# Kernel tuning notes

Measured on AMD Instinct MI355X. Metric: run time of the kernel, lower is better.

Reference implementation:

```python
import jax, jax.numpy as jnp
import numpy as np


def eops_2_to_2(x):
    # x: (N, D, m, m) -> (N, D, 15, m, m), Maron et al. equivariant basis with 'inf' normalization
    m = x.shape[-1]
    fm = float(m)
    eye = jnp.eye(m, dtype=x.dtype)
    diag = jnp.diagonal(x, axis1=-2, axis2=-1)          # (N, D, m)
    sum_diag = diag.sum(-1, keepdims=True)              # (N, D, 1)
    sum_rows = x.sum(-1)                                # (N, D, m) sum over columns j
    sum_cols = x.sum(-2)                                # (N, D, m) sum over rows i
    tot = x.sum((-2, -1))                               # (N, D)

    de = lambda v: v[..., :, None] * eye                # diag_embed (N,D,m) -> (N,D,m,m)
    b_row = lambda v: jnp.broadcast_to(v[..., :, None], v.shape + (m,))           # row i constant = v[i]
    b_col = lambda v: jnp.broadcast_to(v[..., None, :], v.shape[:-1] + (m, m))    # col j constant = v[j]

    op1 = de(diag)
    op2 = de(jnp.broadcast_to(sum_diag, diag.shape)) / fm
    op3 = de(sum_rows) / fm
    op4 = de(sum_cols) / fm
    op5 = de(jnp.broadcast_to(tot[..., None], diag.shape)) / (fm * fm)
    op6 = b_row(sum_cols) / fm
    op7 = b_row(sum_rows) / fm
    op8 = b_col(sum_cols) / fm
    op9 = b_col(sum_rows) / fm
    op10 = x
    op11 = jnp.swapaxes(x, -1, -2)
    op12 = b_row(diag)
    op13 = b_col(diag)
    op14 = jnp.broadcast_to(sum_diag[..., None], x.shape) / fm
    op15 = jnp.broadcast_to(tot[..., None, None], x.shape) / (fm * fm)
    return jnp.stack([op1, op2, op3, op4, op5, op6, op7, op8,
                      op9, op10, op11, op12, op13, op14, op15], axis=2)


def setup_inputs() -> dict:
    key = jax.random.key(0)
    k1, k2 = jax.random.split(key)
    N, D, S, B, m = 32, 32, 32, 15, 128
    std = np.sqrt(2.0 / (D + S + B)).astype(np.float32)
    inputs = jax.random.normal(k1, (N, D, m, m), dtype=jnp.float32)
    coefs = jax.random.normal(k2, (D, S, B), dtype=jnp.float32) * std
    bias = jnp.zeros((1, S, 1, 1), dtype=jnp.float32)
    diag_bias = jnp.zeros((1, S, 1, 1), dtype=jnp.float32)
    return {"inputs": inputs, "coefs": coefs, "bias": bias, "diag_bias": diag_bias}


def reference(inputs, coefs, bias, diag_bias):
    ops = eops_2_to_2(inputs)                               # (N, D, 15, m, m)
    out = jnp.einsum('dsb,ndbij->nsij', coefs, ops)         # (N, S, m, m)
    m = out.shape[-1]
    eye = jnp.eye(m, dtype=out.dtype)[None, None]           # (1,1,m,m)
    return out + bias + eye * diag_bias
```

## Files before the change

### kernel.cpp

```cpp
#include <hip/hip_runtime.h>

#define N_ 32
#define D_ 32
#define S_ 32
#define M_ 128
#define MM_ (M_ * M_)
#define INV_M (1.0f / 128.0f)
#define INV_M2 (1.0f / (128.0f * 128.0f))

typedef float f32x4 __attribute__((ext_vector_type(4)));
typedef __bf16 bf16x8 __attribute__((ext_vector_type(8)));

#define WS_ROWSUM  0
#define WS_COLSUM  131072
#define WS_DIAG    262144
#define WS_SUMDIAG 393216
#define WS_TOT     394240
#define WS_RV      395264
#define WS_CV      526336
#define WS_DG      657408
#define WS_WBF16   788480

__device__ __forceinline__ unsigned short f2bf(float f) {
    unsigned u = __float_as_uint(f);
    u += 0x7fffu + ((u >> 16) & 1u);
    return (unsigned short)(u >> 16);
}

__global__ __launch_bounds__(256) void eq2_reduce(const float* __restrict__ x,
                                                  float* __restrict__ ws) {
    int nd = blockIdx.x;
    int t  = threadIdx.x;
    int g  = t >> 5;
    int j4 = t & 31;

    const float4* xp = (const float4*)(x + (size_t)nd * MM_);

    float* rowsum  = ws + WS_ROWSUM;
    float* colsum  = ws + WS_COLSUM;
    float* diag    = ws + WS_DIAG;
    float* sumdiag = ws + WS_SUMDIAG;
    float* tot     = ws + WS_TOT;

    float4 cs = {0.f, 0.f, 0.f, 0.f};
    float dsum = 0.f, ttot = 0.f;

    for (int r = 0; r < 16; ++r) {
        int i = g * 16 + r;
        float4 v = xp[i * 32 + j4];
        cs.x += v.x; cs.y += v.y; cs.z += v.z; cs.w += v.w;
        float rp = v.x + v.y + v.z + v.w;
        ttot += rp;
        int c = i - 4 * j4;
        if (c >= 0 && c < 4) {
            float dv = (c == 0) ? v.x : (c == 1) ? v.y : (c == 2) ? v.z : v.w;
            diag[nd * M_ + i] = dv;
            dsum += dv;
        }
        float rs = rp;
        for (int msk = 1; msk < 32; msk <<= 1) rs += __shfl_xor(rs, msk, 64);
        if ((t & 31) == 0) rowsum[nd * M_ + i] = rs;
    }

    __shared__ float4 cs_lds[8][32];
    __shared__ float  red[2][4];
    cs_lds[g][j4] = cs;

    for (int msk = 1; msk < 64; msk <<= 1) {
        dsum += __shfl_xor(dsum, msk, 64);
        ttot += __shfl_xor(ttot, msk, 64);
    }
    int wave = t >> 6, lane = t & 63;
    if (lane == 0) { red[0][wave] = dsum; red[1][wave] = ttot; }
    __syncthreads();

    if (t < 32) {
        float4 a = cs_lds[0][t];
        for (int gg = 1; gg < 8; ++gg) {
            float4 b = cs_lds[gg][t];
            a.x += b.x; a.y += b.y; a.z += b.z; a.w += b.w;
        }
        ((float4*)(colsum + nd * M_))[t] = a;
    }
    if (t == 0) {
        sumdiag[nd] = red[0][0] + red[0][1] + red[0][2] + red[0][3];
        tot[nd]     = red[1][0] + red[1][1] + red[1][2] + red[1][3];
    }
}

__global__ __launch_bounds__(128) void eq2_combine(const float* __restrict__ coefs,
                                                   const float* __restrict__ bias,
                                                   const float* __restrict__ diag_bias,
                                                   float* __restrict__ ws) {
    int b = blockIdx.x;
    int n = b >> 5, s = b & 31;
    int i = threadIdx.x;

    const float* rowsum  = ws + WS_ROWSUM;
    const float* colsum  = ws + WS_COLSUM;
    const float* diag    = ws + WS_DIAG;
    const float* sumdiag = ws + WS_SUMDIAG;
    const float* tot     = ws + WS_TOT;

    float rv = 0.f, cv = 0.f, dg = 0.f, kk = 0.f;
    for (int d = 0; d < D_; ++d) {
        const float* cf = coefs + (d * S_ + s) * 15;
        float rs = rowsum[(n * D_ + d) * M_ + i];
        float c2 = colsum[(n * D_ + d) * M_ + i];
        float dv = diag[(n * D_ + d) * M_ + i];
        float sd = sumdiag[n * D_ + d];
        float tt = tot[n * D_ + d];
        rv += (cf[5] * c2 + cf[6] * rs) * INV_M + cf[11] * dv;
        cv += (cf[7] * c2 + cf[8] * rs) * INV_M + cf[12] * dv;
        dg += cf[0] * dv + (cf[1] * sd + cf[2] * rs + cf[3] * c2) * INV_M
              + cf[4] * tt * INV_M2;
        kk += cf[13] * sd * INV_M + cf[14] * tt * INV_M2;
    }
    ws[WS_RV + (n * S_ + s) * M_ + i] = rv + kk + bias[s];
    ws[WS_CV + (n * S_ + s) * M_ + i] = cv;
    ws[WS_DG + (n * S_ + s) * M_ + i] = dg + diag_bias[s];

    if (n == 0 && i < 32) {
        int d = i;
        unsigned short* wsbf = (unsigned short*)(ws + WS_WBF16);
        const float* cf = coefs + (d * S_ + s) * 15;
        wsbf[s * 40 + d]        = f2bf(cf[9]);
        wsbf[(32 + s) * 40 + d] = f2bf(cf[10]);
    }
}

__global__ __launch_bounds__(512, 4) void eq2_main(const float* __restrict__ x,
                                                   const float* __restrict__ ws_,
                                                   float* __restrict__ out) {
    const float* ws = (const float*)__builtin_assume_aligned(ws_, 256);
    int lid = blockIdx.x;
    int n   = (lid & 7) + 8 * (lid >> 8);
    int b   = (lid >> 3) & 31;

    int AR, AC, BR, BC, diagpair;
    if (b < 28) {
        int ti = 0, rem = b;
        while (rem >= 7 - ti) { rem -= 7 - ti; ++ti; }
        int tj = ti + 1 + rem;
        AR = ti * 16; AC = tj * 16;
        BR = tj * 16; BC = ti * 16;
        diagpair = 0;
    } else {
        int p = b - 28;
        AR = AC = (2 * p) * 16;
        BR = BC = (2 * p + 1) * 16;
        diagpair = 1;
    }

    int t    = threadIdx.x;
    int w    = t >> 6;
    int lane = t & 63;
    int lg   = lane >> 4;
    int lj   = lane & 15;

    __shared__ float trf[8 * 545];
    __shared__ float lds_rv[S_][32];
    __shared__ float lds_cv[S_][32];
    __shared__ float lds_dg[S_][32];

    const unsigned short* wsbf = (const unsigned short*)(ws + WS_WBF16);
    const float* xn = x + (size_t)n * (D_ * MM_);

    bf16x8 A10[2], A11[2];
#pragma unroll
    for (int mt = 0; mt < 2; ++mt) {
        A10[mt] = *(const bf16x8*)(wsbf + (mt * 16 + lj) * 40 + lg * 8);
        A11[mt] = *(const bf16x8*)(wsbf + (32 + mt * 16 + lj) * 40 + lg * 8);
    }

    {
        const float* Rv = ws + WS_RV;
        const float* Cv = ws + WS_CV;
        const float* Dg = ws + WS_DG;
#pragma unroll
        for (int k = 0; k < 2; ++k) {
            int idx = k * 512 + t;
            int s = idx >> 5, q = idx & 31;
            int base = (n * S_ + s) * M_;
            int ro = (q < 16) ? AR + q : BR + (q - 16);
            int co = (q < 16) ? AC + q : BC + (q - 16);
            lds_rv[s][q] = Rv[base + ro];
            lds_cv[s][q] = Cv[base + co];
            if (diagpair) lds_dg[s][q] = Dg[base + ro];
        }
    }

    f32x4 aY[4][2], aZ[4][2];
#pragma unroll
    for (int k = 0; k < 4; ++k)
#pragma unroll
        for (int mt = 0; mt < 2; ++mt) { aY[k][mt] = 0.f; aZ[k][mt] = 0.f; }

#pragma unroll
    for (int half = 0; half < 2; ++half) {
        float fv[2][8];
#pragma unroll
        for (int kk = 0; kk < 2; ++kk) {
            int k  = half * 2 + kk;
            int nt = w * 4 + k;
            int tt = nt >> 4, il = nt & 15;
            int Rt = tt ? BR : AR, Ct = tt ? BC : AC;
            const float* src = xn + (Rt + il) * M_ + Ct + lj + (size_t)(lg * 8) * MM_;
#pragma unroll
            for (int e = 0; e < 8; ++e)
                fv[kk][e] = src[(size_t)e * MM_];
        }
#pragma unroll
        for (int kk = 0; kk < 2; ++kk) {
            int k = half * 2 + kk;
            union { unsigned u[4]; bf16x8 v; } cvt;
#pragma unroll
            for (int e = 0; e < 4; ++e)
                cvt.u[e] = (unsigned)f2bf(fv[kk][2 * e]) | ((unsigned)f2bf(fv[kk][2 * e + 1]) << 16);
            bf16x8 Bf = cvt.v;
            aY[k][0] = __builtin_amdgcn_mfma_f32_16x16x32_bf16(A10[0], Bf, aY[k][0], 0, 0, 0);
            aY[k][1] = __builtin_amdgcn_mfma_f32_16x16x32_bf16(A10[1], Bf, aY[k][1], 0, 0, 0);
            aZ[k][0] = __builtin_amdgcn_mfma_f32_16x16x32_bf16(A11[0], Bf, aZ[k][0], 0, 0, 0);
            aZ[k][1] = __builtin_amdgcn_mfma_f32_16x16x32_bf16(A11[1], Bf, aZ[k][1], 0, 0, 0);
        }
    }

#pragma unroll
    for (int r = 0; r < 4; ++r) {
        if (r) __syncthreads();
#pragma unroll
        for (int k = 0; k < 4; ++k) {
            int nt = w * 4 + k;
            int tt = nt >> 4, il = nt & 15;
#pragma unroll
            for (int mt = 0; mt < 2; ++mt)
                trf[(mt * 4 + lg) * 545 + tt * 272 + il * 17 + lj] = aZ[k][mt][r];
        }
        __syncthreads();
#pragma unroll
        for (int k = 0; k < 4; ++k) {
            int nt = w * 4 + k;
            int tt = nt >> 4, il = nt & 15;
            int ttp = diagpair ? tt : 1 - tt;
            int Rt = tt ? BR : AR, Ct = tt ? BC : AC;
#pragma unroll
            for (int mt = 0; mt < 2; ++mt) {
                int s = mt * 16 + 4 * lg + r;
                float zt = trf[(mt * 4 + lg) * 545 + ttp * 272 + lj * 17 + il];
                float o = aY[k][mt][r] + zt + lds_rv[s][tt * 16 + il] + lds_cv[s][tt * 16 + lj];
                if (diagpair && il == lj) o += lds_dg[s][tt * 16 + il];
                out[(size_t)(n * S_ + s) * MM_ + (Rt + il) * M_ + Ct + lj] = o;
            }
        }
    }
}

extern "C" void kernel_launch(void* const* d_in, const int* in_sizes, int n_in,
                              void* d_out, int out_size, void* d_ws, size_t ws_size,
                              hipStream_t stream) {
    const float* x         = (const float*)d_in[0];
    const float* coefs     = (const float*)d_in[1];
    const float* bias      = (const float*)d_in[2];
    const float* diag_bias = (const float*)d_in[3];
    float* out = (float*)d_out;
    float* ws  = (float*)d_ws;

    hipLaunchKernelGGL(eq2_reduce,  dim3(N_ * D_), dim3(256), 0, stream, x, ws);
    hipLaunchKernelGGL(eq2_combine, dim3(N_ * S_), dim3(128), 0, stream, coefs, bias, diag_bias, ws);
    hipLaunchKernelGGL(eq2_main,    dim3(1024), dim3(512), 0, stream, x, ws, out);
}
```

Measured before the change: 53.30 us.

## Fuse reduce, combine and main kernels into one cooperative persistent kernel

Replaces the three kernel launches with a single cooperative kernel of 256 blocks that runs the reduction, the coefficient combine and the MFMA main phase, separated by grid-wide syncs. Each block now handles four tile pairs in a loop and prefetches the next pair's x gather while the current epilogue runs. This removes launch gaps and inter-kernel drains, but cuts the main phase from 1024 blocks to 256 and adds grid-sync overhead. If the cooperative launch fails, it falls back to the three-kernel path.

```diff
diff --git a/kernel.cpp b/kernel.cpp
--- a/kernel.cpp
+++ b/kernel.cpp
@@ -1,4 +1,7 @@
 #include <hip/hip_runtime.h>
+#include <hip/hip_cooperative_groups.h>
+
+namespace cg = cooperative_groups;
 
 #define N_ 32
 #define D_ 32
@@ -25,6 +28,269 @@
     unsigned u = __float_as_uint(f);
     u += 0x7fffu + ((u >> 16) & 1u);
     return (unsigned short)(u >> 16);
+}
+
+__device__ __forceinline__ void decode_pair(int b, int& AR, int& AC, int& BR, int& BC, int& diagpair) {
+    if (b < 28) {
+        int ti = 0, rem = b;
+        while (rem >= 7 - ti) { rem -= 7 - ti; ++ti; }
+        int tj = ti + 1 + rem;
+        AR = ti * 16; AC = tj * 16;
+        BR = tj * 16; BC = ti * 16;
+        diagpair = 0;
+    } else {
+        int p = b - 28;
+        AR = AC = (2 * p) * 16;
+        BR = BC = (2 * p + 1) * 16;
+        diagpair = 1;
+    }
+}
+
+__global__ __launch_bounds__(512, 2) void eq2_fused(const float* __restrict__ x,
+                                                    const float* __restrict__ coefs,
+                                                    const float* __restrict__ bias,
+                                                    const float* __restrict__ diag_bias,
+                                                    float* __restrict__ ws,
+                                                    float* __restrict__ out) {
+    __shared__ __align__(16) unsigned char smem[43008];
+
+    int bid  = blockIdx.x;
+    int xcd  = bid & 7;
+    int u    = bid >> 3;
+    int n    = xcd + 8 * (u >> 3);
+    int sub8 = u & 7;
+    int t    = threadIdx.x;
+
+    cg::grid_group grid = cg::this_grid();
+
+    for (int round = 0; round < 2; ++round) {
+        if (round) __syncthreads();
+
+        float*  rp  = (float*)smem;
+        float4* csl = (float4*)(smem + 33792);
+        float*  dgl = (float*)(smem + 41984);
+
+        int slab = t >> 8, t8 = t & 255;
+        int d  = 4 * sub8 + 2 * round + slab;
+        int nd = n * D_ + d;
+        int g  = t8 >> 5, j4 = t8 & 31;
+        const float4* xp = (const float4*)(x + (size_t)nd * MM_);
+
+        float4 cs = {0.f, 0.f, 0.f, 0.f};
+        for (int r = 0; r < 16; ++r) {
+            int i = g * 16 + r;
+            float4 v = xp[i * 32 + j4];
+            cs.x += v.x; cs.y += v.y; cs.z += v.z; cs.w += v.w;
+            rp[(slab * 128 + i) * 33 + j4] = v.x + v.y + v.z + v.w;
+            int c = i - 4 * j4;
+            if (c >= 0 && c < 4) {
+                float dv = (c == 0) ? v.x : (c == 1) ? v.y : (c == 2) ? v.z : v.w;
+                (ws + WS_DIAG)[nd * M_ + i] = dv;
+                dgl[slab * 128 + i] = dv;
+            }
+        }
+        csl[(slab * 8 + g) * 32 + j4] = cs;
+        __syncthreads();
+
+        if (t8 < 32) {
+            float4 a = csl[(slab * 8) * 32 + t8];
+            for (int gg = 1; gg < 8; ++gg) {
+                float4 b2 = csl[(slab * 8 + gg) * 32 + t8];
+                a.x += b2.x; a.y += b2.y; a.z += b2.z; a.w += b2.w;
+            }
+            ((float4*)((ws + WS_COLSUM) + nd * M_))[t8] = a;
+        }
+        if (t8 < 128) {
+            int r = t8;
+            const float* rowp = rp + (slab * 128 + r) * 33;
+            float rsum = 0.f;
+#pragma unroll
+            for (int k = 0; k < 32; ++k) rsum += rowp[k];
+            (ws + WS_ROWSUM)[nd * M_ + r] = rsum;
+            rp[(slab * 128 + r) * 33 + 32] = rsum;
+        }
+        __syncthreads();
+        if (t8 < 64) {
+            float tt = rp[(slab * 128 + t8) * 33 + 32] + rp[(slab * 128 + t8 + 64) * 33 + 32];
+            float sd = dgl[slab * 128 + t8] + dgl[slab * 128 + t8 + 64];
+            for (int m = 1; m < 64; m <<= 1) {
+                tt += __shfl_xor(tt, m, 64);
+                sd += __shfl_xor(sd, m, 64);
+            }
+            if (t8 == 0) {
+                (ws + WS_TOT)[nd]     = tt;
+                (ws + WS_SUMDIAG)[nd] = sd;
+            }
+        }
+    }
+
+    grid.sync();
+
+    {
+        int s = 4 * sub8 + (t >> 7);
+        int i = t & 127;
+        const float* rowsum  = ws + WS_ROWSUM;
+        const float* colsum  = ws + WS_COLSUM;
+        const float* diag    = ws + WS_DIAG;
+        const float* sumdiag = ws + WS_SUMDIAG;
+        const float* tot     = ws + WS_TOT;
+
+        float rv = 0.f, cv = 0.f, dg = 0.f, kk = 0.f;
+        for (int d = 0; d < D_; ++d) {
+            const float* cf = coefs + (d * S_ + s) * 15;
+            float rs = rowsum[(n * D_ + d) * M_ + i];
+            float c2 = colsum[(n * D_ + d) * M_ + i];
+            float dv = diag[(n * D_ + d) * M_ + i];
+            float sd = sumdiag[n * D_ + d];
+            float tt = tot[n * D_ + d];
+            rv += (cf[5] * c2 + cf[6] * rs) * INV_M + cf[11] * dv;
+            cv += (cf[7] * c2 + cf[8] * rs) * INV_M + cf[12] * dv;
+            dg += cf[0] * dv + (cf[1] * sd + cf[2] * rs + cf[3] * c2) * INV_M
+                  + cf[4] * tt * INV_M2;
+            kk += cf[13] * sd * INV_M + cf[14] * tt * INV_M2;
+        }
+        ws[WS_RV + (n * S_ + s) * M_ + i] = rv + kk + bias[s];
+        ws[WS_CV + (n * S_ + s) * M_ + i] = cv;
+        ws[WS_DG + (n * S_ + s) * M_ + i] = dg + diag_bias[s];
+
+        if (bid < 8 && t < 128) {
+            int ss = 4 * bid + (t >> 5);
+            int d = t & 31;
+            unsigned short* wsbf = (unsigned short*)(ws + WS_WBF16);
+            const float* cf = coefs + (d * S_ + ss) * 15;
+            wsbf[ss * 40 + d]        = f2bf(cf[9]);
+            wsbf[(32 + ss) * 40 + d] = f2bf(cf[10]);
+        }
+    }
+
+    grid.sync();
+
+    {
+        float* trf       = (float*)smem;
+        float (*rvl)[32] = (float(*)[32])(smem + 17440);
+        float (*cvl)[32] = (float(*)[32])(smem + 21536);
+        float (*dgL)[32] = (float(*)[32])(smem + 25632);
+
+        int w    = t >> 6;
+        int lane = t & 63;
+        int lg   = lane >> 4;
+        int lj   = lane & 15;
+
+        const unsigned short* wsbf = (const unsigned short*)(ws + WS_WBF16);
+        const float* xn = x + (size_t)n * (D_ * MM_);
+
+        bf16x8 A10[2], A11[2];
+#pragma unroll
+        for (int mt = 0; mt < 2; ++mt) {
+            A10[mt] = *(const bf16x8*)(wsbf + (mt * 16 + lj) * 40 + lg * 8);
+            A11[mt] = *(const bf16x8*)(wsbf + (32 + mt * 16 + lj) * 40 + lg * 8);
+        }
+
+        auto stage_rv = [&](int AR, int AC, int BR, int BC, int dp) {
+            const float* Rv = ws + WS_RV;
+            const float* Cv = ws + WS_CV;
+            const float* Dg = ws + WS_DG;
+#pragma unroll
+            for (int k = 0; k < 2; ++k) {
+                int idx = k * 512 + t;
+                int s = idx >> 5, qq = idx & 31;
+                int base = (n * S_ + s) * M_;
+                int ro = (qq < 16) ? AR + qq : BR + (qq - 16);
+                int co = (qq < 16) ? AC + qq : BC + (qq - 16);
+                rvl[s][qq] = Rv[base + ro];
+                cvl[s][qq] = Cv[base + co];
+                if (dp) dgL[s][qq] = Dg[base + ro];
+            }
+        };
+        auto gather2 = [&](int AR, int AC, int BR, int BC, int kbase, float fv[2][8]) {
+#pragma unroll
+            for (int kk = 0; kk < 2; ++kk) {
+                int k  = kbase + kk;
+                int nt = w * 4 + k;
+                int tt = nt >> 4, il = nt & 15;
+                int Rt = tt ? BR : AR, Ct = tt ? BC : AC;
+                const float* src = xn + (Rt + il) * M_ + Ct + lj + (size_t)(lg * 8) * MM_;
+#pragma unroll
+                for (int e = 0; e < 8; ++e)
+                    fv[kk][e] = src[(size_t)e * MM_];
+            }
+        };
+        auto mfma2 = [&](float fv[2][8], int kbase, f32x4 aY[4][2], f32x4 aZ[4][2]) {
+#pragma unroll
+            for (int kk = 0; kk < 2; ++kk) {
+                int k = kbase + kk;
+                union { unsigned uu2[4]; bf16x8 v; } cvt;
+#pragma unroll
+                for (int e = 0; e < 4; ++e)
+                    cvt.uu2[e] = (unsigned)f2bf(fv[kk][2 * e]) | ((unsigned)f2bf(fv[kk][2 * e + 1]) << 16);
+                bf16x8 Bf = cvt.v;
+                aY[k][0] = __builtin_amdgcn_mfma_f32_16x16x32_bf16(A10[0], Bf, aY[k][0], 0, 0, 0);
+                aY[k][1] = __builtin_amdgcn_mfma_f32_16x16x32_bf16(A10[1], Bf, aY[k][1], 0, 0, 0);
+                aZ[k][0] = __builtin_amdgcn_mfma_f32_16x16x32_bf16(A11[0], Bf, aZ[k][0], 0, 0, 0);
+                aZ[k][1] = __builtin_amdgcn_mfma_f32_16x16x32_bf16(A11[1], Bf, aZ[k][1], 0, 0, 0);
+            }
+        };
+        auto epilogue = [&](int AR, int AC, int BR, int BC, int dp,
+                            f32x4 aY[4][2], f32x4 aZ[4][2]) {
+#pragma unroll
+            for (int r = 0; r < 4; ++r) {
+                if (r) __syncthreads();
+#pragma unroll
+                for (int k = 0; k < 4; ++k) {
+                    int nt = w * 4 + k;
+                    int tt = nt >> 4, il = nt & 15;
+#pragma unroll
+                    for (int mt = 0; mt < 2; ++mt)
+                        trf[(mt * 4 + lg) * 545 + tt * 272 + il * 17 + lj] = aZ[k][mt][r];
+                }
+                __syncthreads();
+#pragma unroll
+                for (int k = 0; k < 4; ++k) {
+                    int nt = w * 4 + k;
+                    int tt = nt >> 4, il = nt & 15;
+                    int ttp = dp ? tt : 1 - tt;
+                    int Rt = tt ? BR : AR, Ct = tt ? BC : AC;
+#pragma unroll
+                    for (int mt = 0; mt < 2; ++mt) {
+                        int s = mt * 16 + 4 * lg + r;
+                        float zt = trf[(mt * 4 + lg) * 545 + ttp * 272 + lj * 17 + il];
+                        float o = aY[k][mt][r] + zt + rvl[s][tt * 16 + il] + cvl[s][tt * 16 + lj];
+                        if (dp && il == lj) o += dgL[s][tt * 16 + il];
+                        out[(size_t)(n * S_ + s) * MM_ + (Rt + il) * M_ + Ct + lj] = o;
+                    }
+                }
+            }
+        };
+
+        int AR, AC, BR, BC, dp;
+        decode_pair(4 * sub8, AR, AC, BR, BC, dp);
+
+        float fva[2][8];
+        gather2(AR, AC, BR, BC, 0, fva);
+
+        for (int uu = 0; uu < 4; ++uu) {
+            stage_rv(AR, AC, BR, BC, dp);
+            float fvb[2][8];
+            gather2(AR, AC, BR, BC, 2, fvb);
+
+            f32x4 aY[4][2], aZ[4][2];
+#pragma unroll
+            for (int k = 0; k < 4; ++k)
+#pragma unroll
+                for (int mt = 0; mt < 2; ++mt) { aY[k][mt] = 0.f; aZ[k][mt] = 0.f; }
+            mfma2(fva, 0, aY, aZ);
+            mfma2(fvb, 2, aY, aZ);
+
+            int nAR = AR, nAC = AC, nBR = BR, nBC = BC, ndp = dp;
+            if (uu < 3) {
+                decode_pair(4 * sub8 + uu + 1, nAR, nAC, nBR, nBC, ndp);
+                gather2(nAR, nAC, nBR, nBC, 0, fva);
+            }
+            epilogue(AR, AC, BR, BC, dp, aY, aZ);
+            __syncthreads();
+            AR = nAR; AC = nAC; BR = nBR; BC = nBC; dp = ndp;
+        }
+    }
 }
 
 __global__ __launch_bounds__(256) void eq2_reduce(const float* __restrict__ x,
@@ -138,19 +404,7 @@
     int b   = (lid >> 3) & 31;
 
     int AR, AC, BR, BC, diagpair;
-    if (b < 28) {
-        int ti = 0, rem = b;
-        while (rem >= 7 - ti) { rem -= 7 - ti; ++ti; }
-        int tj = ti + 1 + rem;
-        AR = ti * 16; AC = tj * 16;
-        BR = tj * 16; BC = ti * 16;
-        diagpair = 0;
-    } else {
-        int p = b - 28;
-        AR = AC = (2 * p) * 16;
-        BR = BC = (2 * p + 1) * 16;
-        diagpair = 1;
-    }
+    decode_pair(b, AR, AC, BR, BC, diagpair);
 
     int t    = threadIdx.x;
     int w    = t >> 6;
@@ -213,10 +467,10 @@
 #pragma unroll
         for (int kk = 0; kk < 2; ++kk) {
             int k = half * 2 + kk;
-            union { unsigned u[4]; bf16x8 v; } cvt;
+            union { unsigned uu[4]; bf16x8 v; } cvt;
 #pragma unroll
             for (int e = 0; e < 4; ++e)
-                cvt.u[e] = (unsigned)f2bf(fv[kk][2 * e]) | ((unsigned)f2bf(fv[kk][2 * e + 1]) << 16);
+                cvt.uu[e] = (unsigned)f2bf(fv[kk][2 * e]) | ((unsigned)f2bf(fv[kk][2 * e + 1]) << 16);
             bf16x8 Bf = cvt.v;
             aY[k][0] = __builtin_amdgcn_mfma_f32_16x16x32_bf16(A10[0], Bf, aY[k][0], 0, 0, 0);
             aY[k][1] = __builtin_amdgcn_mfma_f32_16x16x32_bf16(A10[1], Bf, aY[k][1], 0, 0, 0);
@@ -265,7 +519,13 @@
     float* out = (float*)d_out;
     float* ws  = (float*)d_ws;
 
-    hipLaunchKernelGGL(eq2_reduce,  dim3(N_ * D_), dim3(256), 0, stream, x, ws);
-    hipLaunchKernelGGL(eq2_combine, dim3(N_ * S_), dim3(128), 0, stream, coefs, bias, diag_bias, ws);
-    hipLaunchKernelGGL(eq2_main,    dim3(1024), dim3(512), 0, stream, x, ws, out);
-}
+    void* args[] = {(void*)&x, (void*)&coefs, (void*)&bias, (void*)&diag_bias,
+                    (void*)&ws, (void*)&out};
+    hipError_t err = hipLaunchCooperativeKernel((const void*)eq2_fused, dim3(256), dim3(512),
+                                                args, 0, stream);
+    if (err != hipSuccess) {
+        hipLaunchKernelGGL(eq2_reduce,  dim3(N_ * D_), dim3(256), 0, stream, x, ws);
+        hipLaunchKernelGGL(eq2_combine, dim3(N_ * S_), dim3(128), 0, stream, coefs, bias, diag_bias, ws);
+        hipLaunchKernelGGL(eq2_main,    dim3(1024), dim3(512), 0, stream, x, ws, out);
+    }
+}
```

Measured after the change: 123.4 us. 2.31x slower.

## Restructure reduce via LDS row sums and drop per-round barriers in main epilogue

Applied to the files above, without the earlier changes.

The reduce kernel now stores partial row sums in shared memory and finishes row, total and diagonal sums with one thread per row instead of per-row shuffle reductions, and it remaps block ids so blocks sharing an n group are scheduled together. The main kernel writes all four accumulator rounds to a larger shared buffer behind a single barrier instead of four barrier rounds. It also drops the LDS staging of row, column and diagonal vectors and reads them directly from global memory in the epilogue. This trades shared-memory occupancy (about 70KB per block) and more global loads for fewer synchronisations.

```diff
diff --git a/kernel.cpp b/kernel.cpp
--- a/kernel.cpp
+++ b/kernel.cpp
@@ -27,64 +27,88 @@
     return (unsigned short)(u >> 16);
 }
 
+__device__ __forceinline__ void decode_pair(int b, int& AR, int& AC, int& BR, int& BC, int& diagpair) {
+    if (b < 28) {
+        int ti = 0, rem = b;
+        while (rem >= 7 - ti) { rem -= 7 - ti; ++ti; }
+        int tj = ti + 1 + rem;
+        AR = ti * 16; AC = tj * 16;
+        BR = tj * 16; BC = ti * 16;
+        diagpair = 0;
+    } else {
+        int p = b - 28;
+        AR = AC = (2 * p) * 16;
+        BR = BC = (2 * p + 1) * 16;
+        diagpair = 1;
+    }
+}
+
 __global__ __launch_bounds__(256) void eq2_reduce(const float* __restrict__ x,
                                                   float* __restrict__ ws) {
-    int nd = blockIdx.x;
+    int lid = blockIdx.x;
+    int n   = (lid & 7) + 8 * (lid >> 8);
+    int d   = (lid >> 3) & 31;
+    int nd  = n * D_ + d;
+
     int t  = threadIdx.x;
     int g  = t >> 5;
     int j4 = t & 31;
 
     const float4* xp = (const float4*)(x + (size_t)nd * MM_);
 
-    float* rowsum  = ws + WS_ROWSUM;
-    float* colsum  = ws + WS_COLSUM;
-    float* diag    = ws + WS_DIAG;
-    float* sumdiag = ws + WS_SUMDIAG;
-    float* tot     = ws + WS_TOT;
+    __shared__ float  rp[128][36];
+    __shared__ float4 csl[8][32];
+    __shared__ float  dgl[128];
 
     float4 cs = {0.f, 0.f, 0.f, 0.f};
-    float dsum = 0.f, ttot = 0.f;
 
     for (int r = 0; r < 16; ++r) {
         int i = g * 16 + r;
         float4 v = xp[i * 32 + j4];
         cs.x += v.x; cs.y += v.y; cs.z += v.z; cs.w += v.w;
-        float rp = v.x + v.y + v.z + v.w;
-        ttot += rp;
+        rp[i][j4] = v.x + v.y + v.z + v.w;
         int c = i - 4 * j4;
         if (c >= 0 && c < 4) {
             float dv = (c == 0) ? v.x : (c == 1) ? v.y : (c == 2) ? v.z : v.w;
-            diag[nd * M_ + i] = dv;
-            dsum += dv;
-        }
-        float rs = rp;
-        for (int msk = 1; msk < 32; msk <<= 1) rs += __shfl_xor(rs, msk, 64);
-        if ((t & 31) == 0) rowsum[nd * M_ + i] = rs;
-    }
-
-    __shared__ float4 cs_lds[8][32];
-    __shared__ float  red[2][4];
-    cs_lds[g][j4] = cs;
-
-    for (int msk = 1; msk < 64; msk <<= 1) {
-        dsum += __shfl_xor(dsum, msk, 64);
-        ttot += __shfl_xor(ttot, msk, 64);
-    }
-    int wave = t >> 6, lane = t & 63;
-    if (lane == 0) { red[0][wave] = dsum; red[1][wave] = ttot; }
+            (ws + WS_DIAG)[nd * M_ + i] = dv;
+            dgl[i] = dv;
+        }
+    }
+    csl[g][j4] = cs;
     __syncthreads();
 
     if (t < 32) {
-        float4 a = cs_lds[0][t];
+        float4 a = csl[0][t];
         for (int gg = 1; gg < 8; ++gg) {
-            float4 b = cs_lds[gg][t];
+            float4 b = csl[gg][t];
             a.x += b.x; a.y += b.y; a.z += b.z; a.w += b.w;
         }
-        ((float4*)(colsum + nd * M_))[t] = a;
-    }
-    if (t == 0) {
-        sumdiag[nd] = red[0][0] + red[0][1] + red[0][2] + red[0][3];
-        tot[nd]     = red[1][0] + red[1][1] + red[1][2] + red[1][3];
+        ((float4*)((ws + WS_COLSUM) + nd * M_))[t] = a;
+    }
+    if (t < 128) {
+        const float4* rowp = (const float4*)rp[t];
+        float4 a = rowp[0];
+#pragma unroll
+        for (int k = 1; k < 8; ++k) {
+            float4 b = rowp[k];
+            a.x += b.x; a.y += b.y; a.z += b.z; a.w += b.w;
+        }
+        float rs = a.x + a.y + a.z + a.w;
+        (ws + WS_ROWSUM)[nd * M_ + t] = rs;
+        rp[t][32] = rs;
+    }
+    __syncthreads();
+    if (t < 64) {
+        float tt = rp[t][32] + rp[t + 64][32];
+        float sd = dgl[t] + dgl[t + 64];
+        for (int m = 1; m < 64; m <<= 1) {
+            tt += __shfl_xor(tt, m, 64);
+            sd += __shfl_xor(sd, m, 64);
+        }
+        if (t == 0) {
+            (ws + WS_TOT)[nd]     = tt;
+            (ws + WS_SUMDIAG)[nd] = sd;
+        }
     }
 }
 
@@ -138,19 +162,7 @@
     int b   = (lid >> 3) & 31;
 
     int AR, AC, BR, BC, diagpair;
-    if (b < 28) {
-        int ti = 0, rem = b;
-        while (rem >= 7 - ti) { rem -= 7 - ti; ++ti; }
-        int tj = ti + 1 + rem;
-        AR = ti * 16; AC = tj * 16;
-        BR = tj * 16; BC = ti * 16;
-        diagpair = 0;
-    } else {
-        int p = b - 28;
-        AR = AC = (2 * p) * 16;
-        BR = BC = (2 * p + 1) * 16;
-        diagpair = 1;
-    }
+    decode_pair(b, AR, AC, BR, BC, diagpair);
 
     int t    = threadIdx.x;
     int w    = t >> 6;
@@ -158,10 +170,7 @@
     int lg   = lane >> 4;
     int lj   = lane & 15;
 
-    __shared__ float trf[8 * 545];
-    __shared__ float lds_rv[S_][32];
-    __shared__ float lds_cv[S_][32];
-    __shared__ float lds_dg[S_][32];
+    __shared__ float zall[4][4360];
 
     const unsigned short* wsbf = (const unsigned short*)(ws + WS_WBF16);
     const float* xn = x + (size_t)n * (D_ * MM_);
@@ -171,23 +180,6 @@
     for (int mt = 0; mt < 2; ++mt) {
         A10[mt] = *(const bf16x8*)(wsbf + (mt * 16 + lj) * 40 + lg * 8);
         A11[mt] = *(const bf16x8*)(wsbf + (32 + mt * 16 + lj) * 40 + lg * 8);
-    }
-
-    {
-        const float* Rv = ws + WS_RV;
-        const float* Cv = ws + WS_CV;
-        const float* Dg = ws + WS_DG;
-#pragma unroll
-        for (int k = 0; k < 2; ++k) {
-            int idx = k * 512 + t;
-            int s = idx >> 5, q = idx & 31;
-            int base = (n * S_ + s) * M_;
-            int ro = (q < 16) ? AR + q : BR + (q - 16);
-            int co = (q < 16) ? AC + q : BC + (q - 16);
-            lds_rv[s][q] = Rv[base + ro];
-            lds_cv[s][q] = Cv[base + co];
-            if (diagpair) lds_dg[s][q] = Dg[base + ro];
-        }
     }
 
     f32x4 aY[4][2], aZ[4][2];
@@ -213,10 +205,10 @@
 #pragma unroll
         for (int kk = 0; kk < 2; ++kk) {
             int k = half * 2 + kk;
-            union { unsigned u[4]; bf16x8 v; } cvt;
+            union { unsigned uu[4]; bf16x8 v; } cvt;
 #pragma unroll
             for (int e = 0; e < 4; ++e)
-                cvt.u[e] = (unsigned)f2bf(fv[kk][2 * e]) | ((unsigned)f2bf(fv[kk][2 * e + 1]) << 16);
+                cvt.uu[e] = (unsigned)f2bf(fv[kk][2 * e]) | ((unsigned)f2bf(fv[kk][2 * e + 1]) << 16);
             bf16x8 Bf = cvt.v;
             aY[k][0] = __builtin_amdgcn_mfma_f32_16x16x32_bf16(A10[0], Bf, aY[k][0], 0, 0, 0);
             aY[k][1] = __builtin_amdgcn_mfma_f32_16x16x32_bf16(A10[1], Bf, aY[k][1], 0, 0, 0);
@@ -226,30 +218,36 @@
     }
 
 #pragma unroll
-    for (int r = 0; r < 4; ++r) {
-        if (r) __syncthreads();
-#pragma unroll
-        for (int k = 0; k < 4; ++k) {
-            int nt = w * 4 + k;
-            int tt = nt >> 4, il = nt & 15;
-#pragma unroll
-            for (int mt = 0; mt < 2; ++mt)
-                trf[(mt * 4 + lg) * 545 + tt * 272 + il * 17 + lj] = aZ[k][mt][r];
-        }
-        __syncthreads();
-#pragma unroll
-        for (int k = 0; k < 4; ++k) {
-            int nt = w * 4 + k;
-            int tt = nt >> 4, il = nt & 15;
-            int ttp = diagpair ? tt : 1 - tt;
-            int Rt = tt ? BR : AR, Ct = tt ? BC : AC;
-#pragma unroll
-            for (int mt = 0; mt < 2; ++mt) {
+    for (int k = 0; k < 4; ++k) {
+        int nt = w * 4 + k;
+        int tt = nt >> 4, il = nt & 15;
+#pragma unroll
+        for (int mt = 0; mt < 2; ++mt)
+#pragma unroll
+            for (int r = 0; r < 4; ++r)
+                zall[r][(mt * 4 + lg) * 545 + tt * 272 + il * 17 + lj] = aZ[k][mt][r];
+    }
+    __syncthreads();
+
+    const float* Rv = ws + WS_RV;
+    const float* Cv = ws + WS_CV;
+    const float* Dg = ws + WS_DG;
+#pragma unroll
+    for (int k = 0; k < 4; ++k) {
+        int nt = w * 4 + k;
+        int tt = nt >> 4, il = nt & 15;
+        int ttp = diagpair ? tt : 1 - tt;
+        int Rt = tt ? BR : AR, Ct = tt ? BC : AC;
+#pragma unroll
+        for (int mt = 0; mt < 2; ++mt) {
+#pragma unroll
+            for (int r = 0; r < 4; ++r) {
                 int s = mt * 16 + 4 * lg + r;
-                float zt = trf[(mt * 4 + lg) * 545 + ttp * 272 + lj * 17 + il];
-                float o = aY[k][mt][r] + zt + lds_rv[s][tt * 16 + il] + lds_cv[s][tt * 16 + lj];
-                if (diagpair && il == lj) o += lds_dg[s][tt * 16 + il];
-                out[(size_t)(n * S_ + s) * MM_ + (Rt + il) * M_ + Ct + lj] = o;
+                int base = (n * S_ + s) * M_;
+                float zt = zall[r][(mt * 4 + lg) * 545 + ttp * 272 + lj * 17 + il];
+                float o = aY[k][mt][r] + zt + Rv[base + Rt + il] + Cv[base + Ct + lj];
+                if (diagpair && il == lj) o += Dg[base + Rt + il];
+                out[(size_t)base * M_ + (Rt + il) * M_ + Ct + lj] = o;
             }
         }
     }
@@ -265,7 +263,7 @@
     float* out = (float*)d_out;
     float* ws  = (float*)d_ws;
 
-    hipLaunchKernelGGL(eq2_reduce,  dim3(N_ * D_), dim3(256), 0, stream, x, ws);
+    hipLaunchKernelGGL(eq2_reduce,  dim3(1024), dim3(256), 0, stream, x, ws);
     hipLaunchKernelGGL(eq2_combine, dim3(N_ * S_), dim3(128), 0, stream, coefs, bias, diag_bias, ws);
     hipLaunchKernelGGL(eq2_main,    dim3(1024), dim3(512), 0, stream, x, ws, out);
 }
```

Result: slower. 59.07 us (+10.8%).
